# Kernel tuning notes

Hardware: AMD Instinct MI355X
Metric: run time of the kernel (lower is better)

Reference implementation:

```python
import jax, jax.numpy as jnp
import numpy as np

BS, DEC, IN_LEN, HID, EMB, VOCAB = 16, 100, 512, 768, 768, 32000


def setup_inputs() -> dict:
    key = jax.random.key(0)
    ks = jax.random.split(key, 8)
    x = jax.random.normal(ks[0], (BS, DEC, HID), dtype=jnp.float32)
    attn_dist = jax.random.normal(ks[1], (BS, DEC, IN_LEN), dtype=jnp.float32)
    enc_input = jax.random.randint(ks[2], (BS, IN_LEN), 0, VOCAB, dtype=jnp.int32)
    enc_output = jax.random.normal(ks[3], (BS, IN_LEN, EMB), dtype=jnp.float32)
    # learned params
    W_vocab = jax.random.normal(ks[4], (HID, VOCAB), dtype=jnp.float32) / np.sqrt(HID)
    b_vocab = jnp.zeros((VOCAB,), dtype=jnp.float32)
    W_gen = jax.random.normal(ks[5], (HID + EMB, 1), dtype=jnp.float32) / np.sqrt(HID + EMB)
    b_gen = jnp.zeros((1,), dtype=jnp.float32)
    return {"x": x, "attn_dist": attn_dist, "enc_input": enc_input,
            "enc_output": enc_output, "W_vocab": W_vocab, "b_vocab": b_vocab,
            "W_gen": W_gen, "b_gen": b_gen}


def reference(x, attn_dist, enc_input, enc_output, W_vocab, b_vocab, W_gen, b_gen):
    # context vector: [bs, dec, emb] = attn @ enc_output
    context = jnp.einsum('bdl,ble->bde', attn_dist, enc_output)
    mix = jnp.concatenate([context, x], axis=2)              # [bs, dec, emb+hid]
    p_gen = jax.nn.sigmoid(mix @ W_gen + b_gen)              # [bs, dec, 1]
    logit = x @ W_vocab + b_vocab                            # [bs, dec, vocab]
    vocab_dist = jax.nn.softmax(logit, axis=2) * p_gen       # [bs, dec, vocab]
    attn_w = jax.nn.softmax(attn_dist, axis=2) * (1.0 - p_gen)  # [bs, dec, in_len]
    # scatter_add attention mass onto vocab ids (duplicate ids accumulate)
    b_idx = jnp.arange(BS)[:, None, None]
    d_idx = jnp.arange(DEC)[None, :, None]
    v_idx = enc_input[:, None, :]                            # broadcast over dec
    mixed = vocab_dist.at[b_idx, d_idx, v_idx].add(attn_w)
    return jnp.log(mixed)
```

## Files before the change

kernel.cpp:

```cpp
#include <hip/hip_runtime.h>
#include <math.h>

#define BS 16
#define DEC 100
#define IN_LEN 512
#define HID 768
#define EMB 768
#define VOCAB 32000
#define NROW (BS*DEC)
#define NTILE_M 13
#define NTILE_N2 125
#define KT2 24
#define A_SHORTS 4096
#define B_SHORTS 8192

using short8 = __attribute__((ext_vector_type(8))) short;
using ushort4v = __attribute__((ext_vector_type(4))) unsigned short;
using f32x4 = __attribute__((ext_vector_type(4))) float;

__device__ __forceinline__ unsigned short f2bf(float f) {
  unsigned u = __float_as_uint(f);
  u = u + 0x7FFFu + ((u >> 16) & 1u);
  return (unsigned short)(u >> 16);
}
__device__ __forceinline__ float bf2f(unsigned short h) {
  return __uint_as_float(((unsigned)h) << 16);
}

__device__ __forceinline__ void gll16(const void* g, void* l) {
  __builtin_amdgcn_global_load_lds(
      (const __attribute__((address_space(1))) unsigned int*)g,
      (__attribute__((address_space(3))) unsigned int*)l, 16, 0, 0);
}

__global__ __launch_bounds__(256) void k0_venc(const float* __restrict__ enc_out,
                                               const float* __restrict__ Wg,
                                               float* __restrict__ venc) {
  int row = blockIdx.x * 4 + (threadIdx.x >> 6);
  int lane = threadIdx.x & 63;
  const float* p = enc_out + (size_t)row * EMB;
  float s = 0.f;
  for (int e = lane; e < EMB; e += 64) s += p[e] * Wg[e];
  for (int off = 32; off; off >>= 1) s += __shfl_xor(s, off);
  if (lane == 0) venc[row] = s;
}

__global__ __launch_bounds__(256) void k1_row(const float* __restrict__ attn,
                                              const float* __restrict__ x,
                                              const float* __restrict__ venc,
                                              const float* __restrict__ Wg,
                                              const float* __restrict__ bgen,
                                              float* __restrict__ pg,
                                              float* __restrict__ lp,
                                              float* __restrict__ m_a,
                                              float* __restrict__ s_a) {
  int r = blockIdx.x;
  int b = r / DEC;
  int tid = threadIdx.x;
  const float* arow = attn + (size_t)r * IN_LEN;
  const float* ve = venc + b * IN_LEN;
  const float* xrow = x + (size_t)r * HID;

  float pdot = 0.f, m = -1e30f;
  for (int l = tid; l < IN_LEN; l += 256) { float a = arow[l]; pdot += a * ve[l]; m = fmaxf(m, a); }
  for (int h = tid; h < HID; h += 256) pdot += xrow[h] * Wg[HID + h];

  for (int off = 32; off; off >>= 1) pdot += __shfl_xor(pdot, off);
  for (int off = 32; off; off >>= 1) m = fmaxf(m, __shfl_xor(m, off));

  __shared__ float red[8];
  if ((tid & 63) == 0) { red[tid >> 6] = pdot; red[4 + (tid >> 6)] = m; }
  __syncthreads();
  float z = red[0] + red[1] + red[2] + red[3];
  m = fmaxf(fmaxf(red[4], red[5]), fmaxf(red[6], red[7]));

  float se = 0.f;
  for (int l = tid; l < IN_LEN; l += 256) se += expf(arow[l] - m);
  for (int off = 32; off; off >>= 1) se += __shfl_xor(se, off);
  __syncthreads();
  if ((tid & 63) == 0) red[tid >> 6] = se;
  __syncthreads();
  se = red[0] + red[1] + red[2] + red[3];

  if (tid == 0) {
    z += bgen[0];
    float p, l_p;
    if (z >= 0.f) { float e = expf(-z); p = 1.f / (1.f + e); l_p = -log1pf(e); }
    else          { float e = expf(z);  p = e / (1.f + e);   l_p = z - log1pf(e); }
    pg[r] = p; lp[r] = l_p; m_a[r] = m; s_a[r] = se;
  }
}

__global__ __launch_bounds__(256) void p0_pack_x(const float* __restrict__ X,
                                                 unsigned short* __restrict__ Xp) {
  int mtile = blockIdx.x, ks = blockIdx.y, tid = threadIdx.x;
  size_t base = ((size_t)(mtile * KT2 + ks)) * A_SHORTS;
#pragma unroll
  for (int i = 0; i < 2; i++) {
    int slot = tid + i * 256;
    int r = slot >> 2, s = slot & 3;
    int row = mtile * 128 + r;
    int k0 = ks * 32 + ((s ^ (r & 3)) << 3);
    short8 v;
    if (row < NROW) {
      const float* p = X + (size_t)row * HID + k0;
#pragma unroll
      for (int j = 0; j < 8; j++) v[j] = (short)f2bf(p[j]);
    } else {
#pragma unroll
      for (int j = 0; j < 8; j++) v[j] = 0;
    }
    *(short8*)&Xp[base + (size_t)slot * 8] = v;
  }
}

__global__ __launch_bounds__(256) void p0_pack_w(const float* __restrict__ W,
                                                 unsigned short* __restrict__ Wp) {
  __shared__ float ld[32][257];
  int ntile = blockIdx.x, ks = blockIdx.y, tid = threadIdx.x;
#pragma unroll
  for (int i = 0; i < 32; i++) {
    int idx = tid + i * 256;
    int kk = idx >> 8, nn = idx & 255;
    ld[kk][nn] = W[(size_t)(ks * 32 + kk) * VOCAB + ntile * 256 + nn];
  }
  __syncthreads();
  size_t base = ((size_t)(ntile * KT2 + ks)) * B_SHORTS;
#pragma unroll
  for (int i = 0; i < 4; i++) {
    int slot = tid + i * 256;
    int n = slot >> 2, s = slot & 3;
    int k0 = (s ^ (n & 3)) << 3;
    short8 v;
#pragma unroll
    for (int j = 0; j < 8; j++) v[j] = (short)f2bf(ld[k0 + j][n]);
    *(short8*)&Wp[base + (size_t)slot * 8] = v;
  }
}

__global__ __launch_bounds__(256, 2) void k2_gemm_v4(const unsigned short* __restrict__ Xp,
                                                     const unsigned short* __restrict__ Wp,
                                                     const float* __restrict__ bvocab,
                                                     float* __restrict__ out,
                                                     unsigned short* __restrict__ lbf,
                                                     float* __restrict__ part,
                                                     int use_bf) {
  __shared__ __align__(16) unsigned short sh[3][12288];

  int bid = blockIdx.x;
  const int NWG = NTILE_M * NTILE_N2;
  const int q = NWG / 8, rr = NWG % 8;
  int xcd = bid & 7, idx = bid >> 3;
  int wg = (xcd < rr ? xcd * (q + 1) : rr * (q + 1) + (xcd - rr) * q) + idx;
  int ntile = wg / NTILE_M, mtile = wg % NTILE_M;

  const int tid = threadIdx.x;
  const int wid = tid >> 6, lane = tid & 63;
  const int wr = wid >> 1, wc = wid & 1;
  const int l15 = lane & 15, hi = lane >> 4;
  const int phys = (hi ^ (l15 & 3)) * 8;

  const unsigned short* aSrc = Xp + (size_t)(mtile * KT2) * A_SHORTS;
  const unsigned short* bSrc = Wp + (size_t)(ntile * KT2) * B_SHORTS;

  const int aoff = (wr * 64 + l15) * 32 + phys;
  const int boff = (wc * 128 + l15) * 32 + phys;

  f32x4 acc[4][8] = {};

#pragma unroll
  for (int t = 0; t < 2; t++) {
    const unsigned short* a = aSrc + (size_t)t * A_SHORTS;
    const unsigned short* b = bSrc + (size_t)t * B_SHORTS;
    unsigned short* dA = &sh[t][0];
    unsigned short* dB = &sh[t][4096];
    gll16(a + (size_t)tid * 8,            dA + tid * 8);
    gll16(a + (size_t)(tid + 256) * 8,    dA + (tid + 256) * 8);
#pragma unroll
    for (int j2 = 0; j2 < 4; j2++)
      gll16(b + (size_t)(tid + j2 * 256) * 8, dB + (tid + j2 * 256) * 8);
  }
  asm volatile("s_waitcnt vmcnt(6)" ::: "memory");
  __builtin_amdgcn_s_barrier();
  asm volatile("" ::: "memory");

  int bcur = 0;
  for (int t = 0; t < KT2; ++t) {
    if (t + 2 < KT2) {
      int bn = bcur + 2; if (bn >= 3) bn -= 3;
      const unsigned short* a = aSrc + (size_t)(t + 2) * A_SHORTS;
      const unsigned short* b = bSrc + (size_t)(t + 2) * B_SHORTS;
      unsigned short* dA = &sh[bn][0];
      unsigned short* dB = &sh[bn][4096];
      gll16(a + (size_t)tid * 8,            dA + tid * 8);
      gll16(a + (size_t)(tid + 256) * 8,    dA + (tid + 256) * 8);
#pragma unroll
      for (int j2 = 0; j2 < 4; j2++)
        gll16(b + (size_t)(tid + j2 * 256) * 8, dB + (tid + j2 * 256) * 8);
    }
    const unsigned short* A = &sh[bcur][0];
    const unsigned short* B = &sh[bcur][4096];
    short8 af[4], bfr[8];
#pragma unroll
    for (int mm = 0; mm < 4; mm++) af[mm] = *(const short8*)&A[aoff + mm * 512];
#pragma unroll
    for (int nn = 0; nn < 8; nn++) bfr[nn] = *(const short8*)&B[boff + nn * 512];
    __builtin_amdgcn_s_setprio(1);
#pragma unroll
    for (int mm = 0; mm < 4; mm++)
#pragma unroll
      for (int nn = 0; nn < 8; nn++)
        acc[mm][nn] = __builtin_amdgcn_mfma_f32_16x16x32_bf16(af[mm], bfr[nn], acc[mm][nn], 0, 0, 0);
    __builtin_amdgcn_s_setprio(0);
    if (t < KT2 - 2) { asm volatile("s_waitcnt vmcnt(6)" ::: "memory"); }
    else             { asm volatile("s_waitcnt vmcnt(0)" ::: "memory"); }
    __builtin_amdgcn_s_barrier();
    asm volatile("" ::: "memory");
    bcur = bcur + 1; if (bcur >= 3) bcur = 0;
  }

  __syncthreads();

  float bb[8];
#pragma unroll
  for (int nn = 0; nn < 8; nn++) bb[nn] = bvocab[ntile * 256 + wc * 128 + nn * 16 + l15];
#pragma unroll
  for (int mm = 0; mm < 4; mm++)
#pragma unroll
    for (int nn = 0; nn < 8; nn++)
#pragma unroll
      for (int j = 0; j < 4; j++) acc[mm][nn][j] += bb[nn];

  unsigned short* ldsC = &sh[0][0];
  float* red = (float*)&sh[2][8192];

  if (use_bf) {
#pragma unroll
    for (int mm = 0; mm < 4; mm++) {
      int row0 = wr * 64 + mm * 16 + hi * 4;
#pragma unroll
      for (int nn = 0; nn < 8; nn++) {
        int col = wc * 128 + nn * 16 + l15;
#pragma unroll
        for (int j = 0; j < 4; j++) ldsC[(row0 + j) * 256 + col] = f2bf(acc[mm][nn][j]);
      }
    }
  } else {
#pragma unroll
    for (int mm = 0; mm < 4; mm++) {
      int row0 = mtile * 128 + wr * 64 + mm * 16 + hi * 4;
#pragma unroll
      for (int nn = 0; nn < 8; nn++) {
        int col = ntile * 256 + wc * 128 + nn * 16 + l15;
#pragma unroll
        for (int j = 0; j < 4; j++) {
          int row = row0 + j;
          if (row < NROW) out[(size_t)row * VOCAB + col] = acc[mm][nn][j];
        }
      }
    }
  }

#pragma unroll
  for (int mm = 0; mm < 4; mm++) {
#pragma unroll
    for (int j = 0; j < 4; j++) {
      float mx = acc[mm][0][j];
#pragma unroll
      for (int nn = 1; nn < 8; nn++) mx = fmaxf(mx, acc[mm][nn][j]);
      mx = fmaxf(mx, __shfl_xor(mx, 1));
      mx = fmaxf(mx, __shfl_xor(mx, 2));
      mx = fmaxf(mx, __shfl_xor(mx, 4));
      mx = fmaxf(mx, __shfl_xor(mx, 8));
      float sl = 0.f;
#pragma unroll
      for (int nn = 0; nn < 8; nn++) sl += __expf(acc[mm][nn][j] - mx);
      sl += __shfl_xor(sl, 1);
      sl += __shfl_xor(sl, 2);
      sl += __shfl_xor(sl, 4);
      sl += __shfl_xor(sl, 8);
      if (l15 == 0) {
        int rloc = wr * 64 + mm * 16 + hi * 4 + j;
        int o = (rloc * 2 + wc) * 2;
        red[o] = mx; red[o + 1] = sl;
      }
    }
  }
  __syncthreads();

  if (use_bf) {
#pragma unroll
    for (int i = 0; i < 16; i++) {
      int flat = tid + i * 256;
      int r = flat >> 5, c = (flat & 31) * 8;
      int grow = mtile * 128 + r;
      if (grow < NROW)
        *(short8*)&lbf[(size_t)grow * VOCAB + ntile * 256 + c] = *(const short8*)&ldsC[r * 256 + c];
    }
  }
  if (tid < 128) {
    int o0 = (tid * 2 + 0) * 2;
    int o1 = (tid * 2 + 1) * 2;
    float m0 = red[o0], s0 = red[o0 + 1];
    float m1 = red[o1], s1 = red[o1 + 1];
    float m = fmaxf(m0, m1);
    float s = s0 * __expf(m0 - m) + s1 * __expf(m1 - m);
    int grow = mtile * 128 + tid;
    if (grow < NROW) {
      part[(size_t)grow * 256 + ntile * 2]     = m;
      part[(size_t)grow * 256 + ntile * 2 + 1] = s;
    }
  }
}

__global__ __launch_bounds__(512) void k4_finish_bf(float* __restrict__ out,
                                                    const unsigned short* __restrict__ lbf,
                                                    const float* __restrict__ part,
                                                    const float* __restrict__ lp) {
  int r = blockIdx.x;
  int tid = threadIdx.x;
  float m = -1e30f, s = 0.f;
  if (tid < NTILE_N2) {
    m = part[(size_t)r * 256 + tid * 2];
    s = part[(size_t)r * 256 + tid * 2 + 1];
  }
  for (int off = 1; off < 64; off <<= 1) {
    float mo = __shfl_xor(m, off), so = __shfl_xor(s, off);
    float nm = fmaxf(m, mo);
    s = s * __expf(m - nm) + so * __expf(mo - nm);
    m = nm;
  }
  __shared__ float sm[8], ss[8], sc[1];
  if ((tid & 63) == 0) { sm[tid >> 6] = m; ss[tid >> 6] = s; }
  __syncthreads();
  if (tid == 0) {
    float mm_ = sm[0], ss_ = ss[0];
    for (int w = 1; w < 8; w++) {
      float nm = fmaxf(mm_, sm[w]);
      ss_ = ss_ * __expf(mm_ - nm) + ss[w] * __expf(sm[w] - nm);
      mm_ = nm;
    }
    sc[0] = lp[r] - (mm_ + __logf(ss_));
  }
  __syncthreads();
  float coef = sc[0];
  const short8* src = (const short8*)(lbf + (size_t)r * VOCAB);
  float* dst = out + (size_t)r * VOCAB;
  for (int i = tid; i < VOCAB / 8; i += 512) {
    short8 v = src[i];
    float4 a, b;
    a.x = bf2f((unsigned short)v[0]) + coef; a.y = bf2f((unsigned short)v[1]) + coef;
    a.z = bf2f((unsigned short)v[2]) + coef; a.w = bf2f((unsigned short)v[3]) + coef;
    b.x = bf2f((unsigned short)v[4]) + coef; b.y = bf2f((unsigned short)v[5]) + coef;
    b.z = bf2f((unsigned short)v[6]) + coef; b.w = bf2f((unsigned short)v[7]) + coef;
    *(float4*)&dst[i * 8]     = a;
    *(float4*)&dst[i * 8 + 4] = b;
  }
}

__global__ __launch_bounds__(256) void k4_finish(float* __restrict__ out,
                                                 const float* __restrict__ part,
                                                 const float* __restrict__ lp) {
  int r = blockIdx.x >> 1, half = blockIdx.x & 1;
  int tid = threadIdx.x;
  float m = -1e30f, s = 0.f;
  if (tid < NTILE_N2) {
    m = part[(size_t)r * 256 + tid * 2];
    s = part[(size_t)r * 256 + tid * 2 + 1];
  }
  for (int off = 1; off < 64; off <<= 1) {
    float mo = __shfl_xor(m, off), so = __shfl_xor(s, off);
    float nm = fmaxf(m, mo);
    s = s * __expf(m - nm) + so * __expf(mo - nm);
    m = nm;
  }
  __shared__ float sm[4], ss[4], sc[1];
  if ((tid & 63) == 0) { sm[tid >> 6] = m; ss[tid >> 6] = s; }
  __syncthreads();
  if (tid == 0) {
    float mm_ = sm[0], ss_ = ss[0];
    for (int w = 1; w < 4; w++) {
      float nm = fmaxf(mm_, sm[w]);
      ss_ = ss_ * __expf(mm_ - nm) + ss[w] * __expf(sm[w] - nm);
      mm_ = nm;
    }
    sc[0] = lp[r] - (mm_ + __logf(ss_));
  }
  __syncthreads();
  float coef = sc[0];
  float4* p = (float4*)(out + (size_t)r * VOCAB + half * (VOCAB / 2));
  for (int i = tid; i < VOCAB / 8; i += 256) {
    float4 v = p[i];
    v.x += coef; v.y += coef; v.z += coef; v.w += coef;
    p[i] = v;
  }
}

__global__ __launch_bounds__(256) void k4_scatter(float* __restrict__ out,
                                                  const float* __restrict__ attn,
                                                  const int* __restrict__ enc,
                                                  const float* __restrict__ pg,
                                                  const float* __restrict__ m_a,
                                                  const float* __restrict__ s_a) {
  int idx = blockIdx.x * 256 + threadIdx.x;
  int l = idx & (IN_LEN - 1);
  int r = idx >> 9;
  int b = r / DEC;
  float omp = 1.f - pg[r];
  if (omp <= 0.f) return;
  float term = omp * expf(attn[(size_t)r * IN_LEN + l] - m_a[r]) / s_a[r];
  int v = enc[b * IN_LEN + l];
  unsigned* ua = (unsigned*)(out + (size_t)r * VOCAB + v);
  unsigned old = *ua;
  while (true) {
    float f = __uint_as_float(old);
    float nf = logf(expf(f) + term);
    unsigned assumed = old;
    old = atomicCAS(ua, assumed, __float_as_uint(nf));
    if (old == assumed) break;
  }
}

#define BM 128
#define BN 128
#define BK 32
__device__ __forceinline__ int swz_old(int row, int k) {
  int slot = (k >> 3) ^ ((row >> 1) & 3);
  return row * 32 + slot * 8 + (k & 7);
}

__global__ __launch_bounds__(256) void k2_gemm_old(const float* __restrict__ X,
                                                   const float* __restrict__ W,
                                                   const float* __restrict__ bvocab,
                                                   float* __restrict__ out) {
  __shared__ __align__(16) unsigned short As[BM * BK];
  __shared__ __align__(16) unsigned short Bs[BN * BK];
  const int mtile = blockIdx.x;
  const int ntile = blockIdx.y;
  const int tid = threadIdx.x;
  const int wid = tid >> 6, lane = tid & 63;
  const int wr = wid >> 1, wc = wid & 1;
  f32x4 acc[4][4] = {};
  float4 areg[4];
  float  breg[16];
  const int nl = tid & 127;
  const int kg = tid >> 7;
  {
#pragma unroll
    for (int i = 0; i < 4; i++) {
      int idx = tid + i * 256;
      int r = mtile * BM + (idx >> 3);
      if (r < NROW) areg[i] = *(const float4*)(X + (size_t)r * HID + (idx & 7) * 4);
      else areg[i] = make_float4(0.f, 0.f, 0.f, 0.f);
    }
    const float* base = W + (size_t)(kg * 16) * VOCAB + ntile * BN + nl;
#pragma unroll
    for (int i = 0; i < 16; i++) breg[i] = base[(size_t)i * VOCAB];
  }
  const int KS = HID / BK;
  for (int ks = 0; ks < KS; ++ks) {
#pragma unroll
    for (int i = 0; i < 4; i++) {
      int idx = tid + i * 256;
      int r = idx >> 3, kq = idx & 7;
      ushort4v w;
      w[0] = f2bf(areg[i].x); w[1] = f2bf(areg[i].y);
      w[2] = f2bf(areg[i].z); w[3] = f2bf(areg[i].w);
      *(ushort4v*)&As[swz_old(r, kq * 4)] = w;
    }
    {
      short8 v0, v1;
#pragma unroll
      for (int i = 0; i < 8; i++) { v0[i] = (short)f2bf(breg[i]); v1[i] = (short)f2bf(breg[8 + i]); }
      *(short8*)&Bs[swz_old(nl, kg * 16)] = v0;
      *(short8*)&Bs[swz_old(nl, kg * 16 + 8)] = v1;
    }
    __syncthreads();
    if (ks + 1 < KS) {
      const int ksn = ks + 1;
#pragma unroll
      for (int i = 0; i < 4; i++) {
        int idx = tid + i * 256;
        int r = mtile * BM + (idx >> 3);
        if (r < NROW) areg[i] = *(const float4*)(X + (size_t)r * HID + ksn * BK + (idx & 7) * 4);
        else areg[i] = make_float4(0.f, 0.f, 0.f, 0.f);
      }
      const float* base = W + (size_t)(ksn * BK + kg * 16) * VOCAB + ntile * BN + nl;
#pragma unroll
      for (int i = 0; i < 16; i++) breg[i] = base[(size_t)i * VOCAB];
    }
    {
      const int k0 = (lane >> 4) * 8;
      const int rbase = wr * 64 + (lane & 15);
      const int cbase = wc * 64 + (lane & 15);
      short8 af[4], bf[4];
#pragma unroll
      for (int mm = 0; mm < 4; mm++) af[mm] = *(const short8*)&As[swz_old(rbase + mm * 16, k0)];
#pragma unroll
      for (int nn = 0; nn < 4; nn++) bf[nn] = *(const short8*)&Bs[swz_old(cbase + nn * 16, k0)];
#pragma unroll
      for (int mm = 0; mm < 4; mm++)
#pragma unroll
        for (int nn = 0; nn < 4; nn++)
          acc[mm][nn] = __builtin_amdgcn_mfma_f32_16x16x32_bf16(af[mm], bf[nn], acc[mm][nn], 0, 0, 0);
    }
    __syncthreads();
  }
#pragma unroll
  for (int mm = 0; mm < 4; mm++) {
    int row0 = mtile * BM + wr * 64 + mm * 16 + (lane >> 4) * 4;
#pragma unroll
    for (int nn = 0; nn < 4; nn++) {
      int col = ntile * BN + wc * 64 + nn * 16 + (lane & 15);
      float bb = bvocab[col];
#pragma unroll
      for (int j = 0; j < 4; j++) {
        int row = row0 + j;
        if (row < NROW) out[(size_t)row * VOCAB + col] = acc[mm][nn][j] + bb;
      }
    }
  }
}

__global__ __launch_bounds__(256) void k3_norm(float* __restrict__ out,
                                               const float* __restrict__ lp) {
  int r = blockIdx.x;
  float4* row = reinterpret_cast<float4*>(out + (size_t)r * VOCAB);
  int tid = threadIdx.x;
  float m = -1e30f, s = 0.f;
  for (int i = tid; i < VOCAB / 4; i += 256) {
    float4 v = row[i];
    float m4 = fmaxf(fmaxf(v.x, v.y), fmaxf(v.z, v.w));
    if (m4 > m) { s *= __expf(m - m4); m = m4; }
    s += __expf(v.x - m) + __expf(v.y - m) + __expf(v.z - m) + __expf(v.w - m);
  }
  for (int off = 32; off; off >>= 1) {
    float mo = __shfl_xor(m, off), so = __shfl_xor(s, off);
    float nm = fmaxf(m, mo);
    s = s * __expf(m - nm) + so * __expf(mo - nm);
    m = nm;
  }
  __shared__ float mred[4], sred[4];
  if ((tid & 63) == 0) { mred[tid >> 6] = m; sred[tid >> 6] = s; }
  __syncthreads();
  if (tid == 0) {
    float mm = mred[0], ss = sred[0];
    for (int w = 1; w < 4; w++) {
      float mo = mred[w], so = sred[w];
      float nm = fmaxf(mm, mo);
      ss = ss * __expf(mm - nm) + so * __expf(mo - nm);
      mm = nm;
    }
    mred[0] = mm; sred[0] = ss;
  }
  __syncthreads();
  m = mred[0]; s = sred[0];
  float coef = lp[r] - (m + __logf(s));
  for (int i = tid; i < VOCAB / 4; i += 256) {
    float4 v = row[i];
    v.x += coef; v.y += coef; v.z += coef; v.w += coef;
    row[i] = v;
  }
}

extern "C" void kernel_launch(void* const* d_in, const int* in_sizes, int n_in,
                              void* d_out, int out_size, void* d_ws, size_t ws_size,
                              hipStream_t stream) {
  (void)in_sizes; (void)n_in; (void)out_size;
  const float* x       = (const float*)d_in[0];
  const float* attn    = (const float*)d_in[1];
  const int*   enc_in  = (const int*)d_in[2];
  const float* enc_out = (const float*)d_in[3];
  const float* Wv      = (const float*)d_in[4];
  const float* bv      = (const float*)d_in[5];
  const float* Wg      = (const float*)d_in[6];
  const float* bg      = (const float*)d_in[7];
  float* out = (float*)d_out;
  float* ws  = (float*)d_ws;

  float* venc = ws;
  float* pg   = ws + 8192;
  float* lp   = ws + 9792;
  float* m_a  = ws + 11392;
  float* s_a  = ws + 12992;
  float* part = ws + 14592;
  unsigned short* Xp = (unsigned short*)(ws + 814592);
  unsigned short* Wp = (unsigned short*)(ws + 1453568);
  unsigned short* Lbf = (unsigned short*)(ws + 13741568);
  const size_t NEED  = (size_t)13741568 * 4;
  const size_t NEED2 = NEED + (size_t)NROW * VOCAB * 2;

  hipLaunchKernelGGL(k0_venc, dim3(2048), dim3(256), 0, stream, enc_out, Wg, venc);
  hipLaunchKernelGGL(k1_row, dim3(NROW), dim3(256), 0, stream, attn, x, venc, Wg, bg,
                     pg, lp, m_a, s_a);

  if (ws_size >= NEED) {
    int use_bf = (ws_size >= NEED2) ? 1 : 0;
    hipLaunchKernelGGL(p0_pack_x, dim3(NTILE_M, KT2), dim3(256), 0, stream, x, Xp);
    hipLaunchKernelGGL(p0_pack_w, dim3(NTILE_N2, KT2), dim3(256), 0, stream, Wv, Wp);
    hipLaunchKernelGGL(k2_gemm_v4, dim3(NTILE_M * NTILE_N2), dim3(256), 0, stream,
                       Xp, Wp, bv, out, Lbf, part, use_bf);
    if (use_bf) {
      hipLaunchKernelGGL(k4_finish_bf, dim3(NROW), dim3(512), 0, stream, out, Lbf, part, lp);
    } else {
      hipLaunchKernelGGL(k4_finish, dim3(NROW * 2), dim3(256), 0, stream, out, part, lp);
    }
    hipLaunchKernelGGL(k4_scatter, dim3((NROW * IN_LEN) / 256), dim3(256), 0, stream,
                       out, attn, enc_in, pg, m_a, s_a);
  } else {
    hipLaunchKernelGGL(k2_gemm_old, dim3(NTILE_M, 250), dim3(256), 0, stream,
                       x, Wv, bv, out);
    hipLaunchKernelGGL(k3_norm, dim3(NROW), dim3(256), 0, stream, out, lp);
    hipLaunchKernelGGL(k4_scatter, dim3((NROW * IN_LEN) / 256), dim3(256), 0, stream,
                       out, attn, enc_in, pg, m_a, s_a);
  }
}
```

Before: 276.8 us.

## Load GEMM fragments directly from global and fuse scatter into finish kernel

The GEMM stops staging A/B tiles through LDS with async global-to-LDS loads and a triple buffer. Each wave now loads its bf16 fragments straight from global memory into registers, double-buffered, and the XOR swizzle in the pack kernels is dropped to match. The scatter-add of attention mass is folded into the bf16 finish kernel as a per-row CAS loop in log space, which removes one launch and a second pass over the output. The trade-offs are that global fragment loads are not shared across waves, so more L2 traffic, and CAS contention on duplicate ids.

```diff
diff --git a/kernel.cpp b/kernel.cpp
--- a/kernel.cpp
+++ b/kernel.cpp
@@ -25,12 +25,6 @@
 }
 __device__ __forceinline__ float bf2f(unsigned short h) {
   return __uint_as_float(((unsigned)h) << 16);
-}
-
-__device__ __forceinline__ void gll16(const void* g, void* l) {
-  __builtin_amdgcn_global_load_lds(
-      (const __attribute__((address_space(1))) unsigned int*)g,
-      (__attribute__((address_space(3))) unsigned int*)l, 16, 0, 0);
 }
 
 __global__ __launch_bounds__(256) void k0_venc(const float* __restrict__ enc_out,
@@ -100,7 +94,7 @@
     int slot = tid + i * 256;
     int r = slot >> 2, s = slot & 3;
     int row = mtile * 128 + r;
-    int k0 = ks * 32 + ((s ^ (r & 3)) << 3);
+    int k0 = ks * 32 + (s << 3);
     short8 v;
     if (row < NROW) {
       const float* p = X + (size_t)row * HID + k0;
@@ -130,7 +124,7 @@
   for (int i = 0; i < 4; i++) {
     int slot = tid + i * 256;
     int n = slot >> 2, s = slot & 3;
-    int k0 = (s ^ (n & 3)) << 3;
+    int k0 = s << 3;
     short8 v;
 #pragma unroll
     for (int j = 0; j < 8; j++) v[j] = (short)f2bf(ld[k0 + j][n]);
@@ -138,14 +132,15 @@
   }
 }
 
-__global__ __launch_bounds__(256, 2) void k2_gemm_v4(const unsigned short* __restrict__ Xp,
-                                                     const unsigned short* __restrict__ Wp,
-                                                     const float* __restrict__ bvocab,
-                                                     float* __restrict__ out,
-                                                     unsigned short* __restrict__ lbf,
-                                                     float* __restrict__ part,
-                                                     int use_bf) {
-  __shared__ __align__(16) unsigned short sh[3][12288];
+__global__ __launch_bounds__(256, 2) void k2_flat(const unsigned short* __restrict__ Xp,
+                                                  const unsigned short* __restrict__ Wp,
+                                                  const float* __restrict__ bvocab,
+                                                  float* __restrict__ out,
+                                                  unsigned short* __restrict__ lbf,
+                                                  float* __restrict__ part,
+                                                  int use_bf) {
+  __shared__ __align__(16) unsigned short ldsC[128 * 256];
+  __shared__ float red[512];
 
   int bid = blockIdx.x;
   const int NWG = NTILE_M * NTILE_N2;
@@ -158,68 +153,40 @@
   const int wid = tid >> 6, lane = tid & 63;
   const int wr = wid >> 1, wc = wid & 1;
   const int l15 = lane & 15, hi = lane >> 4;
-  const int phys = (hi ^ (l15 & 3)) * 8;
 
   const unsigned short* aSrc = Xp + (size_t)(mtile * KT2) * A_SHORTS;
   const unsigned short* bSrc = Wp + (size_t)(ntile * KT2) * B_SHORTS;
 
-  const int aoff = (wr * 64 + l15) * 32 + phys;
-  const int boff = (wc * 128 + l15) * 32 + phys;
+  const int aoff = (wr * 64 + l15) * 32 + hi * 8;
+  const int boff = (wc * 128 + l15) * 32 + hi * 8;
 
   f32x4 acc[4][8] = {};
-
-#pragma unroll
-  for (int t = 0; t < 2; t++) {
-    const unsigned short* a = aSrc + (size_t)t * A_SHORTS;
-    const unsigned short* b = bSrc + (size_t)t * B_SHORTS;
-    unsigned short* dA = &sh[t][0];
-    unsigned short* dB = &sh[t][4096];
-    gll16(a + (size_t)tid * 8,            dA + tid * 8);
-    gll16(a + (size_t)(tid + 256) * 8,    dA + (tid + 256) * 8);
-#pragma unroll
-    for (int j2 = 0; j2 < 4; j2++)
-      gll16(b + (size_t)(tid + j2 * 256) * 8, dB + (tid + j2 * 256) * 8);
-  }
-  asm volatile("s_waitcnt vmcnt(6)" ::: "memory");
-  __builtin_amdgcn_s_barrier();
-  asm volatile("" ::: "memory");
-
-  int bcur = 0;
-  for (int t = 0; t < KT2; ++t) {
-    if (t + 2 < KT2) {
-      int bn = bcur + 2; if (bn >= 3) bn -= 3;
-      const unsigned short* a = aSrc + (size_t)(t + 2) * A_SHORTS;
-      const unsigned short* b = bSrc + (size_t)(t + 2) * B_SHORTS;
-      unsigned short* dA = &sh[bn][0];
-      unsigned short* dB = &sh[bn][4096];
-      gll16(a + (size_t)tid * 8,            dA + tid * 8);
-      gll16(a + (size_t)(tid + 256) * 8,    dA + (tid + 256) * 8);
-#pragma unroll
-      for (int j2 = 0; j2 < 4; j2++)
-        gll16(b + (size_t)(tid + j2 * 256) * 8, dB + (tid + j2 * 256) * 8);
-    }
-    const unsigned short* A = &sh[bcur][0];
-    const unsigned short* B = &sh[bcur][4096];
-    short8 af[4], bfr[8];
-#pragma unroll
-    for (int mm = 0; mm < 4; mm++) af[mm] = *(const short8*)&A[aoff + mm * 512];
-#pragma unroll
-    for (int nn = 0; nn < 8; nn++) bfr[nn] = *(const short8*)&B[boff + nn * 512];
-    __builtin_amdgcn_s_setprio(1);
-#pragma unroll
-    for (int mm = 0; mm < 4; mm++)
-#pragma unroll
-      for (int nn = 0; nn < 8; nn++)
-        acc[mm][nn] = __builtin_amdgcn_mfma_f32_16x16x32_bf16(af[mm], bfr[nn], acc[mm][nn], 0, 0, 0);
-    __builtin_amdgcn_s_setprio(0);
-    if (t < KT2 - 2) { asm volatile("s_waitcnt vmcnt(6)" ::: "memory"); }
-    else             { asm volatile("s_waitcnt vmcnt(0)" ::: "memory"); }
-    __builtin_amdgcn_s_barrier();
-    asm volatile("" ::: "memory");
-    bcur = bcur + 1; if (bcur >= 3) bcur = 0;
-  }
-
-  __syncthreads();
+  short8 aA[4], bA[8], aB[4], bB[8];
+
+#define LOAD_F(adst, bdst, t) { \
+    const unsigned short* ap_ = aSrc + (size_t)(t) * A_SHORTS + aoff; \
+    const unsigned short* bp_ = bSrc + (size_t)(t) * B_SHORTS + boff; \
+    _Pragma("unroll") for (int mm = 0; mm < 4; mm++) adst[mm] = *(const short8*)(ap_ + mm * 512); \
+    _Pragma("unroll") for (int nn = 0; nn < 8; nn++) bdst[nn] = *(const short8*)(bp_ + nn * 512); }
+
+#define MFMA_F(asrcr, bsrcr) { \
+    _Pragma("unroll") for (int mm = 0; mm < 4; mm++) \
+    _Pragma("unroll") for (int nn = 0; nn < 8; nn++) \
+      acc[mm][nn] = __builtin_amdgcn_mfma_f32_16x16x32_bf16(asrcr[mm], bsrcr[nn], acc[mm][nn], 0, 0, 0); }
+
+  LOAD_F(aA, bA, 0);
+  int t = 0;
+  for (; t < KT2 - 2; t += 2) {
+    LOAD_F(aB, bB, t + 1);
+    MFMA_F(aA, bA);
+    LOAD_F(aA, bA, t + 2);
+    MFMA_F(aB, bB);
+  }
+  LOAD_F(aB, bB, KT2 - 1);
+  MFMA_F(aA, bA);
+  MFMA_F(aB, bB);
+#undef LOAD_F
+#undef MFMA_F
 
   float bb[8];
 #pragma unroll
@@ -230,9 +197,6 @@
     for (int nn = 0; nn < 8; nn++)
 #pragma unroll
       for (int j = 0; j < 4; j++) acc[mm][nn][j] += bb[nn];
-
-  unsigned short* ldsC = &sh[0][0];
-  float* red = (float*)&sh[2][8192];
 
   if (use_bf) {
 #pragma unroll
@@ -313,10 +277,15 @@
   }
 }
 
-__global__ __launch_bounds__(512) void k4_finish_bf(float* __restrict__ out,
-                                                    const unsigned short* __restrict__ lbf,
-                                                    const float* __restrict__ part,
-                                                    const float* __restrict__ lp) {
+__global__ __launch_bounds__(512) void k4_fused(float* __restrict__ out,
+                                                const unsigned short* __restrict__ lbf,
+                                                const float* __restrict__ part,
+                                                const float* __restrict__ lp,
+                                                const float* __restrict__ attn,
+                                                const int* __restrict__ enc,
+                                                const float* __restrict__ pg,
+                                                const float* __restrict__ m_a,
+                                                const float* __restrict__ s_a) {
   int r = blockIdx.x;
   int tid = threadIdx.x;
   float m = -1e30f, s = 0.f;
@@ -355,6 +324,24 @@
     b.z = bf2f((unsigned short)v[6]) + coef; b.w = bf2f((unsigned short)v[7]) + coef;
     *(float4*)&dst[i * 8]     = a;
     *(float4*)&dst[i * 8 + 4] = b;
+  }
+  __threadfence();
+  __syncthreads();
+
+  float omp = 1.f - pg[r];
+  if (omp > 0.f && tid < IN_LEN) {
+    int b_ = r / DEC;
+    float term = omp * expf(attn[(size_t)r * IN_LEN + tid] - m_a[r]) / s_a[r];
+    int v = enc[b_ * IN_LEN + tid];
+    unsigned* ua = (unsigned*)(out + (size_t)r * VOCAB + v);
+    unsigned old = *ua;
+    while (true) {
+      float f = __uint_as_float(old);
+      float nf = logf(expf(f) + term);
+      unsigned assumed = old;
+      old = atomicCAS(ua, assumed, __float_as_uint(nf));
+      if (old == assumed) break;
+    }
   }
 }
 
@@ -598,15 +585,16 @@
     int use_bf = (ws_size >= NEED2) ? 1 : 0;
     hipLaunchKernelGGL(p0_pack_x, dim3(NTILE_M, KT2), dim3(256), 0, stream, x, Xp);
     hipLaunchKernelGGL(p0_pack_w, dim3(NTILE_N2, KT2), dim3(256), 0, stream, Wv, Wp);
-    hipLaunchKernelGGL(k2_gemm_v4, dim3(NTILE_M * NTILE_N2), dim3(256), 0, stream,
+    hipLaunchKernelGGL(k2_flat, dim3(NTILE_M * NTILE_N2), dim3(256), 0, stream,
                        Xp, Wp, bv, out, Lbf, part, use_bf);
     if (use_bf) {
-      hipLaunchKernelGGL(k4_finish_bf, dim3(NROW), dim3(512), 0, stream, out, Lbf, part, lp);
+      hipLaunchKernelGGL(k4_fused, dim3(NROW), dim3(512), 0, stream,
+                         out, Lbf, part, lp, attn, enc_in, pg, m_a, s_a);
     } else {
       hipLaunchKernelGGL(k4_finish, dim3(NROW * 2), dim3(256), 0, stream, out, part, lp);
-    }
-    hipLaunchKernelGGL(k4_scatter, dim3((NROW * IN_LEN) / 256), dim3(256), 0, stream,
-                       out, attn, enc_in, pg, m_a, s_a);
+      hipLaunchKernelGGL(k4_scatter, dim3((NROW * IN_LEN) / 256), dim3(256), 0, stream,
+                         out, attn, enc_in, pg, m_a, s_a);
+    }
   } else {
     hipLaunchKernelGGL(k2_gemm_old, dim3(NTILE_M, 250), dim3(256), 0, stream,
                        x, Wv, bv, out);
```

Measured after the change: 996.9 us. 260% more time.

## Fuse attention scatter into finish kernel using shared-memory hash aggregation

Applied to the files above, without the earlier changes.

Merges the separate scatter kernel into the per-row finish kernel. Each block hashes the 512 attention contributions by vocab id into a shared-memory open-addressing table, then applies log(exp(p)+sum) once per unique id after writing the row. This removes a kernel launch and the global atomic/read-modify-write traffic of the scatter, at the cost of extra shared memory, CAS loops and a third barrier in the finish kernel.

```diff
diff --git a/kernel.cpp b/kernel.cpp
--- a/kernel.cpp
+++ b/kernel.cpp
@@ -313,12 +313,23 @@
   }
 }
 
-__global__ __launch_bounds__(512) void k4_finish_bf(float* __restrict__ out,
-                                                    const unsigned short* __restrict__ lbf,
-                                                    const float* __restrict__ part,
-                                                    const float* __restrict__ lp) {
+__global__ __launch_bounds__(512) void k4_fused(float* __restrict__ out,
+                                                const unsigned short* __restrict__ lbf,
+                                                const float* __restrict__ part,
+                                                const float* __restrict__ lp,
+                                                const float* __restrict__ attn,
+                                                const int* __restrict__ enc,
+                                                const float* __restrict__ pg,
+                                                const float* __restrict__ m_a,
+                                                const float* __restrict__ s_a) {
   int r = blockIdx.x;
   int tid = threadIdx.x;
+  __shared__ float sm[8], ss[8], sc[1];
+  __shared__ int   s_key[1024];
+  __shared__ float s_val[1024];
+  s_key[tid] = -1; s_key[tid + 512] = -1;
+  s_val[tid] = 0.f; s_val[tid + 512] = 0.f;
+
   float m = -1e30f, s = 0.f;
   if (tid < NTILE_N2) {
     m = part[(size_t)r * 256 + tid * 2];
@@ -330,7 +341,6 @@
     s = s * __expf(m - nm) + so * __expf(mo - nm);
     m = nm;
   }
-  __shared__ float sm[8], ss[8], sc[1];
   if ((tid & 63) == 0) { sm[tid >> 6] = m; ss[tid >> 6] = s; }
   __syncthreads();
   if (tid == 0) {
@@ -342,8 +352,22 @@
     }
     sc[0] = lp[r] - (mm_ + __logf(ss_));
   }
+
+  float omp = 1.f - pg[r];
+  if (omp > 0.f) {
+    int b_ = r / DEC;
+    float t = omp * __expf(attn[(size_t)r * IN_LEN + tid] - m_a[r]) / s_a[r];
+    int v = enc[b_ * IN_LEN + tid];
+    int slot = v & 1023;
+    while (true) {
+      int old = atomicCAS(&s_key[slot], -1, v);
+      if (old == -1 || old == v) { atomicAdd(&s_val[slot], t); break; }
+      slot = (slot + 1) & 1023;
+    }
+  }
   __syncthreads();
   float coef = sc[0];
+
   const short8* src = (const short8*)(lbf + (size_t)r * VOCAB);
   float* dst = out + (size_t)r * VOCAB;
   for (int i = tid; i < VOCAB / 8; i += 512) {
@@ -355,6 +379,16 @@
     b.z = bf2f((unsigned short)v[6]) + coef; b.w = bf2f((unsigned short)v[7]) + coef;
     *(float4*)&dst[i * 8]     = a;
     *(float4*)&dst[i * 8 + 4] = b;
+  }
+  __syncthreads();
+
+  for (int i = tid; i < 1024; i += 512) {
+    int v = s_key[i];
+    if (v >= 0) {
+      float sum = s_val[i];
+      float p = dst[v];
+      dst[v] = logf(expf(p) + sum);
+    }
   }
 }
 
@@ -601,12 +635,13 @@
     hipLaunchKernelGGL(k2_gemm_v4, dim3(NTILE_M * NTILE_N2), dim3(256), 0, stream,
                        Xp, Wp, bv, out, Lbf, part, use_bf);
     if (use_bf) {
-      hipLaunchKernelGGL(k4_finish_bf, dim3(NROW), dim3(512), 0, stream, out, Lbf, part, lp);
+      hipLaunchKernelGGL(k4_fused, dim3(NROW), dim3(512), 0, stream,
+                         out, Lbf, part, lp, attn, enc_in, pg, m_a, s_a);
     } else {
       hipLaunchKernelGGL(k4_finish, dim3(NROW * 2), dim3(256), 0, stream, out, part, lp);
-    }
-    hipLaunchKernelGGL(k4_scatter, dim3((NROW * IN_LEN) / 256), dim3(256), 0, stream,
-                       out, attn, enc_in, pg, m_a, s_a);
+      hipLaunchKernelGGL(k4_scatter, dim3((NROW * IN_LEN) / 256), dim3(256), 0, stream,
+                         out, attn, enc_in, pg, m_a, s_a);
+    }
   } else {
     hipLaunchKernelGGL(k2_gemm_old, dim3(NTILE_M, 250), dim3(256), 0, stream,
                        x, Wv, bv, out);
```

After: 267.8 us. -3.2%, faster.
